# Performance work log

Measured on AMD Instinct MI355X. Metric: run time of the kernel, lower is better.

## Reference

```python
import jax, jax.numpy as jnp
import numpy as np

B, T, D, H = 8, 1024, 1024, 16
HD = D // H
SCALE = HD ** -0.5


def setup_inputs() -> dict:
    key = jax.random.key(0)
    ks = jax.random.split(key, 5)
    s = 0.02
    return {
        "hidden_states": jax.random.normal(ks[0], (B, T, D), jnp.float32),
        "Wq": jax.random.normal(ks[1], (D, D), jnp.float32) * s,
        "bq": jnp.zeros((D,), jnp.float32),
        "Wk": jax.random.normal(ks[2], (D, D), jnp.float32) * s,
        "bk": jnp.zeros((D,), jnp.float32),
        "Wv": jax.random.normal(ks[3], (D, D), jnp.float32) * s,
        "bv": jnp.zeros((D,), jnp.float32),
        "Wo": jax.random.normal(ks[4], (D, D), jnp.float32) * s,
        "bo": jnp.zeros((D,), jnp.float32),
    }


def _split_heads(x):
    # [B, T, D] -> [B, H, T, HD]
    return x.reshape(B, T, H, HD).transpose(0, 2, 1, 3)


def reference(hidden_states, Wq, bq, Wk, bk, Wv, bv, Wo, bo):
    q = _split_heads((hidden_states @ Wq + bq) * SCALE)
    k = _split_heads(hidden_states @ Wk + bk)
    v = _split_heads(hidden_states @ Wv + bv)
    # [B, H, T, T] attention scores
    scores = jnp.einsum("bhqd,bhkd->bhqk", q, k)
    probs = jax.nn.softmax(scores, axis=-1)
    attn = jnp.einsum("bhqk,bhkd->bhqd", probs, v)
    attn = attn.transpose(0, 2, 1, 3).reshape(B, T, D)
    return attn @ Wo + bo
```

## Files before the change

kernel.cpp:

```cpp
#include <hip/hip_runtime.h>

typedef unsigned short u16;
typedef __attribute__((ext_vector_type(4))) float f32x4;
typedef __attribute__((ext_vector_type(8))) __bf16 bf16x8;
typedef __attribute__((ext_vector_type(4))) __bf16 bf16x4;
typedef __attribute__((ext_vector_type(4))) unsigned short u16x4;
typedef __attribute__((ext_vector_type(8))) unsigned short u16x8;

static __device__ __forceinline__ u16 f2bf(float f) {
    union { float f; unsigned u; } v; v.f = f;
    unsigned r = v.u + 0x7FFFu + ((v.u >> 16) & 1u);
    return (u16)(r >> 16);
}

static __device__ __forceinline__ float exp2f_fast(float x) {
    float r; asm("v_exp_f32 %0, %1" : "=v"(r) : "v"(x)); return r;
}

static __device__ __forceinline__ void gload16(const u16* g, u16* l) {
    __builtin_amdgcn_global_load_lds(
        (const __attribute__((address_space(1))) unsigned int*)g,
        (__attribute__((address_space(3))) unsigned int*)l, 16, 0, 0);
}

template<int N> static __device__ __forceinline__ void vm_wait() {
    if constexpr (N >= 8)      asm volatile("s_waitcnt vmcnt(8)" ::: "memory");
    else if constexpr (N == 6) asm volatile("s_waitcnt vmcnt(6)" ::: "memory");
    else if constexpr (N == 4) asm volatile("s_waitcnt vmcnt(4)" ::: "memory");
    else if constexpr (N == 3) asm volatile("s_waitcnt vmcnt(3)" ::: "memory");
    else                       asm volatile("s_waitcnt vmcnt(0)" ::: "memory");
}

#define SWZ64(row, ec) (((row) * 64) + ((((ec) ^ ((row) & 7))) << 3))

__global__ __launch_bounds__(256) void k_cvt(const float* __restrict__ in, u16* __restrict__ out) {
    size_t i = (size_t)blockIdx.x * 256 + threadIdx.x;
    float4 v = ((const float4*)in)[i];
    u16x4 o; o[0] = f2bf(v.x); o[1] = f2bf(v.y); o[2] = f2bf(v.z); o[3] = f2bf(v.w);
    *(u16x4*)(out + i * 4) = o;
}

__global__ __launch_bounds__(256) void k_wtrans4(
    const float* __restrict__ W0, const float* __restrict__ W1,
    const float* __restrict__ W2, const float* __restrict__ W3,
    u16* __restrict__ T0, u16* __restrict__ T1, u16* __restrict__ T2, u16* __restrict__ T3,
    float s0) {
    const float* W; u16* Tt; float sc;
    switch (blockIdx.z) {
        case 0:  W = W0; Tt = T0; sc = s0;  break;
        case 1:  W = W1; Tt = T1; sc = 1.f; break;
        case 2:  W = W2; Tt = T2; sc = 1.f; break;
        default: W = W3; Tt = T3; sc = 1.f; break;
    }
    __shared__ float tile[32][33];
    int n0 = blockIdx.x * 32, k0 = blockIdx.y * 32;
    int tid = threadIdx.x;
    int r = tid >> 3, c = (tid & 7) * 4;
    float4 v = *(const float4*)(W + (size_t)(k0 + r) * 1024 + n0 + c);
    tile[r][c] = v.x; tile[r][c + 1] = v.y; tile[r][c + 2] = v.z; tile[r][c + 3] = v.w;
    __syncthreads();
    u16x4 o;
    o[0] = f2bf(tile[c][r] * sc);
    o[1] = f2bf(tile[c + 1][r] * sc);
    o[2] = f2bf(tile[c + 2][r] * sc);
    o[3] = f2bf(tile[c + 3][r] * sc);
    *(u16x4*)(Tt + (size_t)(n0 + r) * 1024 + k0 + c) = o;
}

template<int BN>
__global__ __launch_bounds__(512, 2) void k_g256(
    const u16* __restrict__ A, const u16* __restrict__ Bt,
    const float* __restrict__ bias, const float* __restrict__ biasK, float qscale,
    u16* __restrict__ obf, u16* __restrict__ obK, float* __restrict__ of32,
    int ldc, int bias_row, int nblk, int mode) {
    constexpr int WN = (BN == 256) ? 4 : 2;
    constexpr int WAVE_M = (BN == 256) ? 128 : 64;
    constexpr int M_REP = WAVE_M / 16;
    constexpr int ABUF = 256 * 64;
    constexpr int BBUF = BN * 64;
    __shared__ u16 As[2 * ABUF];
    __shared__ u16 Bs[2 * BBUF];
    const int tid = threadIdx.x;
    const int l = tid & 63, w = tid >> 6;
    const int mw = w / WN, nw = w % WN;
    const int fr = l & 15, gg = l >> 4, f4 = gg * 4;
    const int id = blockIdx.x;
    const int swz = (id & 7) * 32 + (id >> 3);
    const int bm = swz / nblk, bn = swz % nblk;
    const size_t m0 = (size_t)bm * 256, n0v = (size_t)bn * BN;

    const int strow = tid >> 3;
    const int sch = ((tid & 7) ^ (strow & 7)) * 8;
    const u16* Ag = A + (m0 + strow) * 1024 + sch;
    const u16* Bg = Bt + (n0v + strow) * 1024 + sch;
    const int ldst = tid * 8;

    const int kc0 = (gg ^ (fr & 7)) << 3;
    const int abase = (mw * WAVE_M + fr) * 64;
    const int bbase = (nw * 64 + fr) * 64;

    f32x4 acc[M_REP][4] = {};

#define SA(c, J, b) gload16(Ag + (size_t)(c) * 65536 + (size_t)(J) * 64, As + (b) * ABUF + (c) * 4096 + ldst);
#define SB(c, J, b) gload16(Bg + (size_t)(c) * 65536 + (size_t)(J) * 64, Bs + (b) * BBUF + (c) * 4096 + ldst);
#define PH_BAR()                                                        \
    __builtin_amdgcn_s_barrier();                                       \
    asm volatile("s_waitcnt lgkmcnt(0)" ::: "memory");                  \
    __builtin_amdgcn_sched_barrier(0)
#define MFMA16(AB)                                                      \
    __builtin_amdgcn_s_setprio(1);                                      \
    _Pragma("unroll")                                                   \
    for (int mt = 0; mt < 4; ++mt)                                      \
        _Pragma("unroll")                                               \
        for (int nt = 0; nt < 4; ++nt)                                  \
            acc[(AB) + mt][nt] = __builtin_amdgcn_mfma_f32_16x16x32_bf16(afr[mt], bfr[nt], acc[(AB) + mt][nt], 0, 0, 0); \
    __builtin_amdgcn_s_setprio(0)

    SA(0, 0, 0) SA(1, 0, 0) SA(2, 0, 0) SA(3, 0, 0)
    SB(0, 0, 0) SB(1, 0, 0)
    if constexpr (BN == 256) { SB(2, 0, 0) SB(3, 0, 0) }

#define GT256(b, J, STG)                                                                      \
    {                                                                                         \
        asm volatile("s_waitcnt vmcnt(0)" ::: "memory");                                      \
        __builtin_amdgcn_s_barrier();                                                         \
        bf16x8 bfr[4], afr[4];                                                                \
        _Pragma("unroll")                                                                     \
        for (int nt = 0; nt < 4; ++nt) bfr[nt] = *(const bf16x8*)(&Bs[(b) * BBUF + bbase + nt * 1024 + kc0]); \
        _Pragma("unroll")                                                                     \
        for (int mt = 0; mt < 4; ++mt) afr[mt] = *(const bf16x8*)(&As[(b) * ABUF + abase + mt * 1024 + kc0]); \
        if (STG) { SA(0, (J) + 1, (b) ^ 1) SA(1, (J) + 1, (b) ^ 1) }                          \
        PH_BAR();                                                                             \
        MFMA16(0);                                                                            \
        _Pragma("unroll")                                                                     \
        for (int mt = 0; mt < 4; ++mt) afr[mt] = *(const bf16x8*)(&As[(b) * ABUF + abase + (mt + 4) * 1024 + kc0]); \
        if (STG) { SA(2, (J) + 1, (b) ^ 1) SA(3, (J) + 1, (b) ^ 1) }                          \
        PH_BAR();                                                                             \
        MFMA16(4);                                                                            \
        _Pragma("unroll")                                                                     \
        for (int nt = 0; nt < 4; ++nt) bfr[nt] = *(const bf16x8*)(&Bs[(b) * BBUF + bbase + nt * 1024 + (kc0 ^ 32)]); \
        _Pragma("unroll")                                                                     \
        for (int mt = 0; mt < 4; ++mt) afr[mt] = *(const bf16x8*)(&As[(b) * ABUF + abase + mt * 1024 + (kc0 ^ 32)]); \
        if (STG) { SB(0, (J) + 1, (b) ^ 1) SB(1, (J) + 1, (b) ^ 1) }                          \
        PH_BAR();                                                                             \
        MFMA16(0);                                                                            \
        _Pragma("unroll")                                                                     \
        for (int mt = 0; mt < 4; ++mt) afr[mt] = *(const bf16x8*)(&As[(b) * ABUF + abase + (mt + 4) * 1024 + (kc0 ^ 32)]); \
        if (STG) { SB(2, (J) + 1, (b) ^ 1) SB(3, (J) + 1, (b) ^ 1) }                          \
        PH_BAR();                                                                             \
        MFMA16(4);                                                                            \
    }

#define GT128(b, J, STG)                                                                      \
    {                                                                                         \
        asm volatile("s_waitcnt vmcnt(0)" ::: "memory");                                      \
        __builtin_amdgcn_s_barrier();                                                         \
        bf16x8 bfr[4], afr[4];                                                                \
        _Pragma("unroll")                                                                     \
        for (int nt = 0; nt < 4; ++nt) bfr[nt] = *(const bf16x8*)(&Bs[(b) * BBUF + bbase + nt * 1024 + kc0]); \
        _Pragma("unroll")                                                                     \
        for (int mt = 0; mt < 4; ++mt) afr[mt] = *(const bf16x8*)(&As[(b) * ABUF + abase + mt * 1024 + kc0]); \
        if (STG) { SA(0, (J) + 1, (b) ^ 1) SA(1, (J) + 1, (b) ^ 1) SB(0, (J) + 1, (b) ^ 1) }  \
        PH_BAR();                                                                             \
        MFMA16(0);                                                                            \
        _Pragma("unroll")                                                                     \
        for (int nt = 0; nt < 4; ++nt) bfr[nt] = *(const bf16x8*)(&Bs[(b) * BBUF + bbase + nt * 1024 + (kc0 ^ 32)]); \
        _Pragma("unroll")                                                                     \
        for (int mt = 0; mt < 4; ++mt) afr[mt] = *(const bf16x8*)(&As[(b) * ABUF + abase + mt * 1024 + (kc0 ^ 32)]); \
        if (STG) { SA(2, (J) + 1, (b) ^ 1) SA(3, (J) + 1, (b) ^ 1) SB(1, (J) + 1, (b) ^ 1) }  \
        PH_BAR();                                                                             \
        MFMA16(0);                                                                            \
    }

    if constexpr (BN == 256) {
#pragma unroll 1
        for (int j = 0; j < 14; j += 2) { GT256(0, j, 1) GT256(1, j + 1, 1) }
        GT256(0, 14, 1) GT256(1, 15, 0)
    } else {
#pragma unroll 1
        for (int j = 0; j < 14; j += 2) { GT128(0, j, 1) GT128(1, j + 1, 1) }
        GT128(0, 14, 1) GT128(1, 15, 0)
    }
#undef GT256
#undef GT128
#undef SA
#undef SB
#undef PH_BAR
#undef MFMA16

    const int mrow0 = (int)m0 + mw * WAVE_M;
    const int ncol0 = (int)n0v + nw * 64;
    if (mode == 1) {
#pragma unroll
        for (int mt = 0; mt < M_REP; ++mt)
#pragma unroll
            for (int nt = 0; nt < 4; ++nt) {
                const int col = ncol0 + nt * 16 + fr;
                const int seg = col >> 10, colm = col & 1023;
                const float bb = (seg ? biasK[colm] : bias[colm] * qscale);
                u16* op = seg ? obK : obf;
#pragma unroll
                for (int r = 0; r < 4; ++r)
                    op[(size_t)(mrow0 + mt * 16 + f4 + r) * 1024 + colm] = f2bf(acc[mt][nt][r] + bb);
            }
    } else if (mode == 2) {
#pragma unroll
        for (int mt = 0; mt < M_REP; ++mt) {
            float rb_[4];
#pragma unroll
            for (int r = 0; r < 4; ++r) rb_[r] = bias[mrow0 + mt * 16 + f4 + r];
#pragma unroll
            for (int nt = 0; nt < 4; ++nt) {
                const int col = ncol0 + nt * 16 + fr;
                const int colp = (col & ~31) | (((col >> 2) & 3) << 3) |
                                 (((col >> 4) & 1) << 2) | (col & 3);
#pragma unroll
                for (int r = 0; r < 4; ++r) {
                    const size_t row = (size_t)(mrow0 + mt * 16 + f4 + r);
                    obf[row * (size_t)ldc + colp] = f2bf(acc[mt][nt][r] + rb_[r]);
                }
            }
        }
    } else {
#pragma unroll
        for (int mt = 0; mt < M_REP; ++mt) {
            float rb_[4];
#pragma unroll
            for (int r = 0; r < 4; ++r)
                rb_[r] = bias_row ? bias[mrow0 + mt * 16 + f4 + r] : 0.f;
#pragma unroll
            for (int nt = 0; nt < 4; ++nt) {
                const int col = ncol0 + nt * 16 + fr;
                const float cb = bias_row ? 0.f : bias[col];
#pragma unroll
                for (int r = 0; r < 4; ++r) {
                    const size_t row = (size_t)(mrow0 + mt * 16 + f4 + r);
                    const float vv = acc[mt][nt][r] + cb + rb_[r];
                    if (of32) of32[row * (size_t)ldc + col] = vv;
                    else      obf[row * (size_t)ldc + col] = f2bf(vv);
                }
            }
        }
    }
}

static __device__ __forceinline__ void qk_tile(const u16* Ks, int fr, int gg,
                                               bf16x8 qA0, bf16x8 qA1, bf16x8 qB0, bf16x8 qB1,
                                               float mA, float mB, f32x4 sA[4], f32x4 sB[4]) {
    __builtin_amdgcn_s_setprio(1);
#pragma unroll
    for (int nt = 0; nt < 4; ++nt) {
        const int rk = nt * 16 + fr;
        const bf16x8 kf0 = *(const bf16x8*)(&Ks[SWZ64(rk, gg)]);
        const bf16x8 kf1 = *(const bf16x8*)(&Ks[SWZ64(rk, gg + 4)]);
        f32x4 z = {-mA, -mA, -mA, -mA};
        z = __builtin_amdgcn_mfma_f32_16x16x32_bf16(kf0, qA0, z, 0, 0, 0);
        z = __builtin_amdgcn_mfma_f32_16x16x32_bf16(kf1, qA1, z, 0, 0, 0);
        sA[nt] = z;
        f32x4 y = {-mB, -mB, -mB, -mB};
        y = __builtin_amdgcn_mfma_f32_16x16x32_bf16(kf0, qB0, y, 0, 0, 0);
        y = __builtin_amdgcn_mfma_f32_16x16x32_bf16(kf1, qB1, y, 0, 0, 0);
        sB[nt] = y;
    }
    __builtin_amdgcn_s_setprio(0);
}

static __device__ __forceinline__ void sm_tile(const f32x4 s[4], f32x4 o[4],
                                               float& m, float& lsum, bf16x4 p[4]) {
    float mymax = s[0][0];
#pragma unroll
    for (int nt = 0; nt < 4; ++nt)
#pragma unroll
        for (int r = 0; r < 4; ++r) mymax = fmaxf(mymax, s[nt][r]);
    float ps = 0.f;
#pragma unroll
    for (int nt = 0; nt < 4; ++nt)
#pragma unroll
        for (int r = 0; r < 4; ++r) {
            const float pp = exp2f_fast(s[nt][r]);
            ps += pp; p[nt][r] = (__bf16)pp;
        }
    if (__builtin_expect(__any(mymax > 11.0f), 0)) {
        float rm = fmaxf(mymax, __shfl_xor(mymax, 16, 64));
        rm = fmaxf(rm, __shfl_xor(rm, 32, 64));
        const float d = fmaxf(rm, 0.f);
        const float fac = exp2f_fast(-d);
        m += d; lsum *= fac;
#pragma unroll
        for (int mt = 0; mt < 4; ++mt)
#pragma unroll
            for (int r = 0; r < 4; ++r) o[mt][r] *= fac;
        ps = 0.f;
#pragma unroll
        for (int nt = 0; nt < 4; ++nt)
#pragma unroll
            for (int r = 0; r < 4; ++r) {
                const float pp = exp2f_fast(s[nt][r] - d);
                ps += pp; p[nt][r] = (__bf16)pp;
            }
    }
    lsum += ps;
}

static __device__ __forceinline__ void pv_tile(const u16* Vs, int fr, int gg,
                                               const bf16x4 pA[4], const bf16x4 pB[4],
                                               f32x4 oA[4], f32x4 oB[4]) {
    const bf16x8 BA0 = __builtin_shufflevector(pA[0], pA[1], 0, 1, 2, 3, 4, 5, 6, 7);
    const bf16x8 BA1 = __builtin_shufflevector(pA[2], pA[3], 0, 1, 2, 3, 4, 5, 6, 7);
    const bf16x8 BB0 = __builtin_shufflevector(pB[0], pB[1], 0, 1, 2, 3, 4, 5, 6, 7);
    const bf16x8 BB1 = __builtin_shufflevector(pB[2], pB[3], 0, 1, 2, 3, 4, 5, 6, 7);
    __builtin_amdgcn_s_setprio(1);
#pragma unroll
    for (int mt = 0; mt < 4; ++mt) {
        const int rv = mt * 16 + fr;
        const bf16x8 vk0 = *(const bf16x8*)(&Vs[SWZ64(rv, gg)]);
        const bf16x8 vk1 = *(const bf16x8*)(&Vs[SWZ64(rv, gg + 4)]);
        oA[mt] = __builtin_amdgcn_mfma_f32_16x16x32_bf16(vk0, BA0, oA[mt], 0, 0, 0);
        oA[mt] = __builtin_amdgcn_mfma_f32_16x16x32_bf16(vk1, BA1, oA[mt], 0, 0, 0);
        oB[mt] = __builtin_amdgcn_mfma_f32_16x16x32_bf16(vk0, BB0, oB[mt], 0, 0, 0);
        oB[mt] = __builtin_amdgcn_mfma_f32_16x16x32_bf16(vk1, BB1, oB[mt], 0, 0, 0);
    }
    __builtin_amdgcn_s_setprio(0);
}

__global__ __launch_bounds__(256, 2) void k_flash(const u16* __restrict__ Q, const u16* __restrict__ K,
                                                  const u16* __restrict__ Vt2, u16* __restrict__ O) {
    __shared__ u16 Ks[4][64 * 64];
    __shared__ u16 Vs[4][64 * 64];
    const int tid = threadIdx.x;
    const int l = tid & 63, w = tid >> 6;
    const int id = blockIdx.x;
    const int swz = (id & 7) * 128 + (id >> 3);
    const int bh = swz >> 3, qt = swz & 7;
    const int b = bh >> 4, h = bh & 15;
    const int qw = qt * 128 + w * 32;
    const int fr = l & 15, gg = l >> 4, f4 = gg * 4, f8 = gg * 8;

    const u16* qpA = Q + ((size_t)(b * 1024 + qw + fr)) * 1024 + h * 64 + f8;
    const u16* qpB = qpA + 16 * 1024;
    const bf16x8 qA0 = *(const bf16x8*)qpA;
    const bf16x8 qA1 = *(const bf16x8*)(qpA + 32);
    const bf16x8 qB0 = *(const bf16x8*)qpB;
    const bf16x8 qB1 = *(const bf16x8*)(qpB + 32);

    const int jj0 = w * 2, jj1 = w * 2 + 1;
    const int sr0 = jj0 * 8 + (l >> 3), sr1 = jj1 * 8 + (l >> 3);
    const int sc = ((l & 7) ^ (l >> 3)) * 8;
    const u16* kg0 = K + ((size_t)(b * 1024 + sr0)) * 1024 + h * 64 + sc;
    const u16* kg1 = K + ((size_t)(b * 1024 + sr1)) * 1024 + h * 64 + sc;
    const u16* vg0 = Vt2 + ((size_t)(h * 64 + sr0)) * 8192 + b * 1024 + sc;
    const u16* vg1 = Vt2 + ((size_t)(h * 64 + sr1)) * 8192 + b * 1024 + sc;
    const int lk0 = jj0 * 512 + l * 8, lk1 = jj1 * 512 + l * 8;

#define FSTG(S, kt)                                         \
    gload16(kg0 + (size_t)(kt) * 1024, Ks[S] + lk0);        \
    gload16(kg1 + (size_t)(kt) * 1024, Ks[S] + lk1);        \
    gload16(vg0 + (kt), Vs[S] + lk0);                       \
    gload16(vg1 + (kt), Vs[S] + lk1);

    f32x4 oA[4] = {}, oB[4] = {};
    float mA = 0.f, lA = 0.f, mB = 0.f, lB = 0.f;
    bf16x4 p0A[4], p0B[4], p1A[4], p1B[4];

    FSTG(0, 0) FSTG(1, 64)

#define FITER(T, PCA, PCB, PPA, PPB, VMN, DOPV)                              \
    {                                                                        \
        vm_wait<VMN>();                                                      \
        __builtin_amdgcn_s_barrier();                                        \
        f32x4 sA[4], sB[4];                                                  \
        qk_tile(Ks[(T) & 3], fr, gg, qA0, qA1, qB0, qB1, mA, mB, sA, sB);    \
        if ((T) + 2 <= 15) { FSTG((((T) + 2) & 3), ((T) + 2) * 64) }         \
        if (DOPV) pv_tile(Vs[((T) - 1) & 3], fr, gg, PPA, PPB, oA, oB);      \
        sm_tile(sA, oA, mA, lA, PCA);                                        \
        sm_tile(sB, oB, mB, lB, PCB);                                        \
    }

    FITER(0,  p0A, p0B, p1A, p1B, 4, false)
    FITER(1,  p1A, p1B, p0A, p0B, 4, true)
    FITER(2,  p0A, p0B, p1A, p1B, 4, true)
    FITER(3,  p1A, p1B, p0A, p0B, 4, true)
    FITER(4,  p0A, p0B, p1A, p1B, 4, true)
    FITER(5,  p1A, p1B, p0A, p0B, 4, true)
    FITER(6,  p0A, p0B, p1A, p1B, 4, true)
    FITER(7,  p1A, p1B, p0A, p0B, 4, true)
    FITER(8,  p0A, p0B, p1A, p1B, 4, true)
    FITER(9,  p1A, p1B, p0A, p0B, 4, true)
    FITER(10, p0A, p0B, p1A, p1B, 4, true)
    FITER(11, p1A, p1B, p0A, p0B, 4, true)
    FITER(12, p0A, p0B, p1A, p1B, 4, true)
    FITER(13, p1A, p1B, p0A, p0B, 4, true)
    FITER(14, p0A, p0B, p1A, p1B, 4, true)
    FITER(15, p1A, p1B, p0A, p0B, 0, true)
#undef FITER
#undef FSTG
    pv_tile(Vs[3], fr, gg, p1A, p1B, oA, oB);

    lA += __shfl_xor(lA, 16, 64); lA += __shfl_xor(lA, 32, 64);
    lB += __shfl_xor(lB, 16, 64); lB += __shfl_xor(lB, 32, 64);
    const float ivA = 1.0f / lA, ivB = 1.0f / lB;
    u16* opA = O + ((size_t)(b * 1024 + qw + fr)) * 1024 + h * 64;
    u16* opB = opA + 16 * 1024;
#pragma unroll
    for (int mt = 0; mt < 4; ++mt) {
        u16x4 oa, ob;
#pragma unroll
        for (int r = 0; r < 4; ++r) { oa[r] = f2bf(oA[mt][r] * ivA); ob[r] = f2bf(oB[mt][r] * ivB); }
        *(u16x4*)(opA + mt * 16 + f4) = oa;
        *(u16x4*)(opB + mt * 16 + f4) = ob;
    }
}

extern "C" void kernel_launch(void* const* d_in, const int* in_sizes, int n_in,
                              void* d_out, int out_size, void* d_ws, size_t ws_size,
                              hipStream_t stream) {
    (void)in_sizes; (void)n_in; (void)out_size; (void)ws_size;
    const float* hs = (const float*)d_in[0];
    const float* Wq = (const float*)d_in[1];
    const float* bq = (const float*)d_in[2];
    const float* Wk = (const float*)d_in[3];
    const float* bk = (const float*)d_in[4];
    const float* Wv = (const float*)d_in[5];
    const float* bv = (const float*)d_in[6];
    const float* Wo = (const float*)d_in[7];
    const float* bo = (const float*)d_in[8];
    float* out = (float*)d_out;
    char* ws = (char*)d_ws;
    const size_t MB = 1024ull * 1024ull;
    u16* Xb  = (u16*)(ws);
    u16* Wqt = (u16*)(ws + 16 * MB);
    u16* Wkt = (u16*)(ws + 18 * MB);
    u16* Wvt = (u16*)(ws + 20 * MB);
    u16* Wot = (u16*)(ws + 22 * MB);
    u16* Qb  = (u16*)(ws + 24 * MB);
    u16* Kb  = (u16*)(ws + 40 * MB);
    u16* Vt2 = (u16*)(ws + 56 * MB);
    u16* Ob  = Xb;

    const float SCALE_Q = 0.125f * 1.4426950408889634f;

    k_cvt<<<dim3(8192), dim3(256), 0, stream>>>(hs, Xb);
    k_wtrans4<<<dim3(32, 32, 4), dim3(256), 0, stream>>>(Wq, Wk, Wv, Wo, Wqt, Wkt, Wvt, Wot, SCALE_Q);
    k_g256<256><<<dim3(256), dim3(512), 0, stream>>>(Xb, Wqt, bq, bk, SCALE_Q,
                                                     Qb, Kb, nullptr, 1024, 0, 8, 1);
    k_g256<128><<<dim3(256), dim3(512), 0, stream>>>(Wvt, Xb, bv, nullptr, 1.f,
                                                     Vt2, nullptr, nullptr, 8192, 1, 64, 2);
    k_flash<<<dim3(1024), dim3(256), 0, stream>>>(Qb, Kb, Vt2, Ob);
    k_g256<128><<<dim3(256), dim3(512), 0, stream>>>(Ob, Wot, bo, nullptr, 1.f,
                                                     nullptr, nullptr, out, 1024, 0, 8, 0);
}
```

Measured before the change: 153.7 us.

## Split GEMM K-tiles into half planes and stagger K/V loads in flash

The projection GEMM now stores each 64-wide K tile as two 32-wide LDS planes with a new swizzle. It waits only for the first half-plane before starting MFMAs, using partial vmcnt waits in place of a full vmcnt(0) drain. The flash attention kernel cuts its K/V ring from four stages to three and loads V one tile later than K, which lowers LDS use and lets loads overlap compute. The risks are subtle waitcnt and buffer-index mistakes, plus the 32-wide plane layout changing LDS bank behaviour.

```diff
diff --git a/kernel.cpp b/kernel.cpp
--- a/kernel.cpp
+++ b/kernel.cpp
@@ -28,6 +28,7 @@
     else if constexpr (N == 6) asm volatile("s_waitcnt vmcnt(6)" ::: "memory");
     else if constexpr (N == 4) asm volatile("s_waitcnt vmcnt(4)" ::: "memory");
     else if constexpr (N == 3) asm volatile("s_waitcnt vmcnt(3)" ::: "memory");
+    else if constexpr (N == 2) asm volatile("s_waitcnt vmcnt(2)" ::: "memory");
     else                       asm volatile("s_waitcnt vmcnt(0)" ::: "memory");
 }
 
@@ -76,8 +77,10 @@
     constexpr int WN = (BN == 256) ? 4 : 2;
     constexpr int WAVE_M = (BN == 256) ? 128 : 64;
     constexpr int M_REP = WAVE_M / 16;
-    constexpr int ABUF = 256 * 64;
-    constexpr int BBUF = BN * 64;
+    constexpr int APLANE = 256 * 32;
+    constexpr int ABUF = 2 * APLANE;
+    constexpr int BPLANE = BN * 32;
+    constexpr int BBUF = 2 * BPLANE;
     __shared__ u16 As[2 * ABUF];
     __shared__ u16 Bs[2 * BBUF];
     const int tid = threadIdx.x;
@@ -89,21 +92,21 @@
     const int bm = swz / nblk, bn = swz % nblk;
     const size_t m0 = (size_t)bm * 256, n0v = (size_t)bn * BN;
 
-    const int strow = tid >> 3;
-    const int sch = ((tid & 7) ^ (strow & 7)) * 8;
-    const u16* Ag = A + (m0 + strow) * 1024 + sch;
-    const u16* Bg = Bt + (n0v + strow) * 1024 + sch;
-    const int ldst = tid * 8;
-
-    const int kc0 = (gg ^ (fr & 7)) << 3;
-    const int abase = (mw * WAVE_M + fr) * 64;
-    const int bbase = (nw * 64 + fr) * 64;
+    const u16* AgS = A + (m0 + (tid >> 2)) * 1024 + ((tid & 3) ^ ((tid >> 3) & 3)) * 8;
+    const u16* BgS = Bt + (n0v + (tid >> 2)) * 1024 + ((tid & 3) ^ ((tid >> 3) & 3)) * 8;
+    const int t8 = tid * 8;
+
+    const int kcsw = (gg ^ ((fr >> 1) & 3)) * 8;
+    const int arow = mw * WAVE_M + fr;
+    const int brow = nw * 64 + fr;
 
     f32x4 acc[M_REP][4] = {};
 
-#define SA(c, J, b) gload16(Ag + (size_t)(c) * 65536 + (size_t)(J) * 64, As + (b) * ABUF + (c) * 4096 + ldst);
-#define SB(c, J, b) gload16(Bg + (size_t)(c) * 65536 + (size_t)(J) * 64, Bs + (b) * BBUF + (c) * 4096 + ldst);
-#define PH_BAR()                                                        \
+#define SA(hr, kh, TJ, b) gload16(AgS + (hr) * 131072 + (TJ) * 64 + (kh) * 32, \
+                                  As + (b) * ABUF + (kh) * APLANE + (hr) * 4096 + t8);
+#define SB(hr, kh, TJ, b) gload16(BgS + (hr) * 131072 + (TJ) * 64 + (kh) * 32, \
+                                  Bs + (b) * BBUF + (kh) * BPLANE + (hr) * 4096 + t8);
+#define PH_END()                                                        \
     __builtin_amdgcn_s_barrier();                                       \
     asm volatile("s_waitcnt lgkmcnt(0)" ::: "memory");                  \
     __builtin_amdgcn_sched_barrier(0)
@@ -116,76 +119,84 @@
             acc[(AB) + mt][nt] = __builtin_amdgcn_mfma_f32_16x16x32_bf16(afr[mt], bfr[nt], acc[(AB) + mt][nt], 0, 0, 0); \
     __builtin_amdgcn_s_setprio(0)
 
-    SA(0, 0, 0) SA(1, 0, 0) SA(2, 0, 0) SA(3, 0, 0)
-    SB(0, 0, 0) SB(1, 0, 0)
-    if constexpr (BN == 256) { SB(2, 0, 0) SB(3, 0, 0) }
-
-#define GT256(b, J, STG)                                                                      \
+    if constexpr (BN == 256) {
+        SA(0, 0, 0, 0) SA(1, 0, 0, 0) SB(0, 0, 0, 0) SB(1, 0, 0, 0)
+        SA(0, 1, 0, 0) SA(1, 1, 0, 0) SB(0, 1, 0, 0) SB(1, 1, 0, 0)
+    } else {
+        SA(0, 0, 0, 0) SA(1, 0, 0, 0) SB(0, 0, 0, 0)
+        SA(0, 1, 0, 0) SA(1, 1, 0, 0) SB(0, 1, 0, 0)
+    }
+
+#define GT256(b, J, STG, VM3)                                                                 \
     {                                                                                         \
-        asm volatile("s_waitcnt vmcnt(0)" ::: "memory");                                      \
+        vm_wait<4>();                                                                         \
         __builtin_amdgcn_s_barrier();                                                         \
         bf16x8 bfr[4], afr[4];                                                                \
         _Pragma("unroll")                                                                     \
-        for (int nt = 0; nt < 4; ++nt) bfr[nt] = *(const bf16x8*)(&Bs[(b) * BBUF + bbase + nt * 1024 + kc0]); \
-        _Pragma("unroll")                                                                     \
-        for (int mt = 0; mt < 4; ++mt) afr[mt] = *(const bf16x8*)(&As[(b) * ABUF + abase + mt * 1024 + kc0]); \
-        if (STG) { SA(0, (J) + 1, (b) ^ 1) SA(1, (J) + 1, (b) ^ 1) }                          \
-        PH_BAR();                                                                             \
+        for (int nt = 0; nt < 4; ++nt) bfr[nt] = *(const bf16x8*)(&Bs[(b) * BBUF + (brow + nt * 16) * 32 + kcsw]); \
+        _Pragma("unroll")                                                                     \
+        for (int mt = 0; mt < 4; ++mt) afr[mt] = *(const bf16x8*)(&As[(b) * ABUF + (arow + mt * 16) * 32 + kcsw]); \
+        if (STG) { SA(0, 0, (J) + 1, (b) ^ 1) SA(1, 0, (J) + 1, (b) ^ 1) }                    \
+        PH_END();                                                                             \
         MFMA16(0);                                                                            \
         _Pragma("unroll")                                                                     \
-        for (int mt = 0; mt < 4; ++mt) afr[mt] = *(const bf16x8*)(&As[(b) * ABUF + abase + (mt + 4) * 1024 + kc0]); \
-        if (STG) { SA(2, (J) + 1, (b) ^ 1) SA(3, (J) + 1, (b) ^ 1) }                          \
-        PH_BAR();                                                                             \
+        for (int mt = 0; mt < 4; ++mt) afr[mt] = *(const bf16x8*)(&As[(b) * ABUF + (arow + (mt + 4) * 16) * 32 + kcsw]); \
+        if (STG) { SB(0, 0, (J) + 1, (b) ^ 1) SB(1, 0, (J) + 1, (b) ^ 1) }                    \
+        PH_END();                                                                             \
         MFMA16(4);                                                                            \
-        _Pragma("unroll")                                                                     \
-        for (int nt = 0; nt < 4; ++nt) bfr[nt] = *(const bf16x8*)(&Bs[(b) * BBUF + bbase + nt * 1024 + (kc0 ^ 32)]); \
-        _Pragma("unroll")                                                                     \
-        for (int mt = 0; mt < 4; ++mt) afr[mt] = *(const bf16x8*)(&As[(b) * ABUF + abase + mt * 1024 + (kc0 ^ 32)]); \
-        if (STG) { SB(0, (J) + 1, (b) ^ 1) SB(1, (J) + 1, (b) ^ 1) }                          \
-        PH_BAR();                                                                             \
+        vm_wait<VM3>();                                                                       \
+        __builtin_amdgcn_s_barrier();                                                         \
+        _Pragma("unroll")                                                                     \
+        for (int nt = 0; nt < 4; ++nt) bfr[nt] = *(const bf16x8*)(&Bs[(b) * BBUF + BPLANE + (brow + nt * 16) * 32 + kcsw]); \
+        _Pragma("unroll")                                                                     \
+        for (int mt = 0; mt < 4; ++mt) afr[mt] = *(const bf16x8*)(&As[(b) * ABUF + APLANE + (arow + mt * 16) * 32 + kcsw]); \
+        if (STG) { SA(0, 1, (J) + 1, (b) ^ 1) SA(1, 1, (J) + 1, (b) ^ 1) }                    \
+        PH_END();                                                                             \
         MFMA16(0);                                                                            \
         _Pragma("unroll")                                                                     \
-        for (int mt = 0; mt < 4; ++mt) afr[mt] = *(const bf16x8*)(&As[(b) * ABUF + abase + (mt + 4) * 1024 + (kc0 ^ 32)]); \
-        if (STG) { SB(2, (J) + 1, (b) ^ 1) SB(3, (J) + 1, (b) ^ 1) }                          \
-        PH_BAR();                                                                             \
+        for (int mt = 0; mt < 4; ++mt) afr[mt] = *(const bf16x8*)(&As[(b) * ABUF + APLANE + (arow + (mt + 4) * 16) * 32 + kcsw]); \
+        if (STG) { SB(0, 1, (J) + 1, (b) ^ 1) SB(1, 1, (J) + 1, (b) ^ 1) }                    \
+        PH_END();                                                                             \
         MFMA16(4);                                                                            \
     }
 
-#define GT128(b, J, STG)                                                                      \
+#define GT128(b, J, STG, VM2)                                                                 \
     {                                                                                         \
-        asm volatile("s_waitcnt vmcnt(0)" ::: "memory");                                      \
+        vm_wait<3>();                                                                         \
         __builtin_amdgcn_s_barrier();                                                         \
         bf16x8 bfr[4], afr[4];                                                                \
         _Pragma("unroll")                                                                     \
-        for (int nt = 0; nt < 4; ++nt) bfr[nt] = *(const bf16x8*)(&Bs[(b) * BBUF + bbase + nt * 1024 + kc0]); \
-        _Pragma("unroll")                                                                     \
-        for (int mt = 0; mt < 4; ++mt) afr[mt] = *(const bf16x8*)(&As[(b) * ABUF + abase + mt * 1024 + kc0]); \
-        if (STG) { SA(0, (J) + 1, (b) ^ 1) SA(1, (J) + 1, (b) ^ 1) SB(0, (J) + 1, (b) ^ 1) }  \
-        PH_BAR();                                                                             \
+        for (int nt = 0; nt < 4; ++nt) bfr[nt] = *(const bf16x8*)(&Bs[(b) * BBUF + (brow + nt * 16) * 32 + kcsw]); \
+        _Pragma("unroll")                                                                     \
+        for (int mt = 0; mt < 4; ++mt) afr[mt] = *(const bf16x8*)(&As[(b) * ABUF + (arow + mt * 16) * 32 + kcsw]); \
+        if (STG) { SA(0, 0, (J) + 1, (b) ^ 1) SA(1, 0, (J) + 1, (b) ^ 1) SB(0, 0, (J) + 1, (b) ^ 1) } \
+        PH_END();                                                                             \
         MFMA16(0);                                                                            \
-        _Pragma("unroll")                                                                     \
-        for (int nt = 0; nt < 4; ++nt) bfr[nt] = *(const bf16x8*)(&Bs[(b) * BBUF + bbase + nt * 1024 + (kc0 ^ 32)]); \
-        _Pragma("unroll")                                                                     \
-        for (int mt = 0; mt < 4; ++mt) afr[mt] = *(const bf16x8*)(&As[(b) * ABUF + abase + mt * 1024 + (kc0 ^ 32)]); \
-        if (STG) { SA(2, (J) + 1, (b) ^ 1) SA(3, (J) + 1, (b) ^ 1) SB(1, (J) + 1, (b) ^ 1) }  \
-        PH_BAR();                                                                             \
+        vm_wait<VM2>();                                                                       \
+        __builtin_amdgcn_s_barrier();                                                         \
+        _Pragma("unroll")                                                                     \
+        for (int nt = 0; nt < 4; ++nt) bfr[nt] = *(const bf16x8*)(&Bs[(b) * BBUF + BPLANE + (brow + nt * 16) * 32 + kcsw]); \
+        _Pragma("unroll")                                                                     \
+        for (int mt = 0; mt < 4; ++mt) afr[mt] = *(const bf16x8*)(&As[(b) * ABUF + APLANE + (arow + mt * 16) * 32 + kcsw]); \
+        if (STG) { SA(0, 1, (J) + 1, (b) ^ 1) SA(1, 1, (J) + 1, (b) ^ 1) SB(0, 1, (J) + 1, (b) ^ 1) } \
+        PH_END();                                                                             \
         MFMA16(0);                                                                            \
     }
 
     if constexpr (BN == 256) {
 #pragma unroll 1
-        for (int j = 0; j < 14; j += 2) { GT256(0, j, 1) GT256(1, j + 1, 1) }
-        GT256(0, 14, 1) GT256(1, 15, 0)
+        for (int j = 0; j < 14; j += 2) { GT256(0, j, 1, 4) GT256(1, j + 1, 1, 4) }
+        GT256(0, 14, 1, 4) GT256(1, 15, 0, 0)
     } else {
 #pragma unroll 1
-        for (int j = 0; j < 14; j += 2) { GT128(0, j, 1) GT128(1, j + 1, 1) }
-        GT128(0, 14, 1) GT128(1, 15, 0)
+        for (int j = 0; j < 14; j += 2) { GT128(0, j, 1, 3) GT128(1, j + 1, 1, 3) }
+        GT128(0, 14, 1, 3) GT128(1, 15, 0, 0)
     }
 #undef GT256
 #undef GT128
 #undef SA
 #undef SB
-#undef PH_BAR
+#undef PH_END
 #undef MFMA16
 
     const int mrow0 = (int)m0 + mw * WAVE_M;
@@ -325,8 +336,8 @@
 
 __global__ __launch_bounds__(256, 2) void k_flash(const u16* __restrict__ Q, const u16* __restrict__ K,
                                                   const u16* __restrict__ Vt2, u16* __restrict__ O) {
-    __shared__ u16 Ks[4][64 * 64];
-    __shared__ u16 Vs[4][64 * 64];
+    __shared__ u16 Ks[3][64 * 64];
+    __shared__ u16 Vs[3][64 * 64];
     const int tid = threadIdx.x;
     const int l = tid & 63, w = tid >> 6;
     const int id = blockIdx.x;
@@ -352,9 +363,10 @@
     const u16* vg1 = Vt2 + ((size_t)(h * 64 + sr1)) * 8192 + b * 1024 + sc;
     const int lk0 = jj0 * 512 + l * 8, lk1 = jj1 * 512 + l * 8;
 
-#define FSTG(S, kt)                                         \
+#define FSTGK(S, kt)                                        \
     gload16(kg0 + (size_t)(kt) * 1024, Ks[S] + lk0);        \
-    gload16(kg1 + (size_t)(kt) * 1024, Ks[S] + lk1);        \
+    gload16(kg1 + (size_t)(kt) * 1024, Ks[S] + lk1);
+#define FSTGV(S, kt)                                        \
     gload16(vg0 + (kt), Vs[S] + lk0);                       \
     gload16(vg1 + (kt), Vs[S] + lk1);
 
@@ -362,39 +374,43 @@
     float mA = 0.f, lA = 0.f, mB = 0.f, lB = 0.f;
     bf16x4 p0A[4], p0B[4], p1A[4], p1B[4];
 
-    FSTG(0, 0) FSTG(1, 64)
-
-#define FITER(T, PCA, PCB, PPA, PPB, VMN, DOPV)                              \
+    FSTGK(0, 0) FSTGK(1, 64) FSTGV(0, 0)
+
+#define FITER(T, QS, PS, KS, VS, PCA, PCB, PPA, PPB, VMN, DOPV, DOK, DOV)    \
     {                                                                        \
         vm_wait<VMN>();                                                      \
         __builtin_amdgcn_s_barrier();                                        \
         f32x4 sA[4], sB[4];                                                  \
-        qk_tile(Ks[(T) & 3], fr, gg, qA0, qA1, qB0, qB1, mA, mB, sA, sB);    \
-        if ((T) + 2 <= 15) { FSTG((((T) + 2) & 3), ((T) + 2) * 64) }         \
-        if (DOPV) pv_tile(Vs[((T) - 1) & 3], fr, gg, PPA, PPB, oA, oB);      \
+        qk_tile(Ks[QS], fr, gg, qA0, qA1, qB0, qB1, mA, mB, sA, sB);         \
+        if (DOK) { FSTGK(KS, ((T) + 2) * 64) }                               \
+        if (DOV) { FSTGV(VS, ((T) + 1) * 64) }                               \
+        if (DOPV) pv_tile(Vs[PS], fr, gg, PPA, PPB, oA, oB);                 \
         sm_tile(sA, oA, mA, lA, PCA);                                        \
         sm_tile(sB, oB, mB, lB, PCB);                                        \
     }
 
-    FITER(0,  p0A, p0B, p1A, p1B, 4, false)
-    FITER(1,  p1A, p1B, p0A, p0B, 4, true)
-    FITER(2,  p0A, p0B, p1A, p1B, 4, true)
-    FITER(3,  p1A, p1B, p0A, p0B, 4, true)
-    FITER(4,  p0A, p0B, p1A, p1B, 4, true)
-    FITER(5,  p1A, p1B, p0A, p0B, 4, true)
-    FITER(6,  p0A, p0B, p1A, p1B, 4, true)
-    FITER(7,  p1A, p1B, p0A, p0B, 4, true)
-    FITER(8,  p0A, p0B, p1A, p1B, 4, true)
-    FITER(9,  p1A, p1B, p0A, p0B, 4, true)
-    FITER(10, p0A, p0B, p1A, p1B, 4, true)
-    FITER(11, p1A, p1B, p0A, p0B, 4, true)
-    FITER(12, p0A, p0B, p1A, p1B, 4, true)
-    FITER(13, p1A, p1B, p0A, p0B, 4, true)
-    FITER(14, p0A, p0B, p1A, p1B, 4, true)
-    FITER(15, p1A, p1B, p0A, p0B, 0, true)
+    FITER(0,  0, 0, 2, 1, p0A, p0B, p1A, p1B, 4, 0, 1, 1)
+    FITER(1,  1, 0, 0, 2, p1A, p1B, p0A, p0B, 4, 1, 1, 1)
+    FITER(2,  2, 1, 1, 0, p0A, p0B, p1A, p1B, 4, 1, 1, 1)
+    FITER(3,  0, 2, 2, 1, p1A, p1B, p0A, p0B, 4, 1, 1, 1)
+    FITER(4,  1, 0, 0, 2, p0A, p0B, p1A, p1B, 4, 1, 1, 1)
+    FITER(5,  2, 1, 1, 0, p1A, p1B, p0A, p0B, 4, 1, 1, 1)
+    FITER(6,  0, 2, 2, 1, p0A, p0B, p1A, p1B, 4, 1, 1, 1)
+    FITER(7,  1, 0, 0, 2, p1A, p1B, p0A, p0B, 4, 1, 1, 1)
+    FITER(8,  2, 1, 1, 0, p0A, p0B, p1A, p1B, 4, 1, 1, 1)
+    FITER(9,  0, 2, 2, 1, p1A, p1B, p0A, p0B, 4, 1, 1, 1)
+    FITER(10, 1, 0, 0, 2, p0A, p0B, p1A, p1B, 4, 1, 1, 1)
+    FITER(11, 2, 1, 1, 0, p1A, p1B, p0A, p0B, 4, 1, 1, 1)
+    FITER(12, 0, 2, 2, 1, p0A, p0B, p1A, p1B, 4, 1, 1, 1)
+    FITER(13, 1, 0, 0, 2, p1A, p1B, p0A, p0B, 4, 1, 1, 1)
+    FITER(14, 2, 1, 0, 0, p0A, p0B, p1A, p1B, 4, 1, 0, 1)
+    FITER(15, 0, 2, 0, 0, p1A, p1B, p0A, p0B, 2, 1, 0, 0)
 #undef FITER
-#undef FSTG
-    pv_tile(Vs[3], fr, gg, p1A, p1B, oA, oB);
+    vm_wait<0>();
+    __builtin_amdgcn_s_barrier();
+    pv_tile(Vs[0], fr, gg, p1A, p1B, oA, oB);
+#undef FSTGK
+#undef FSTGV
 
     lA += __shfl_xor(lA, 16, 64); lA += __shfl_xor(lA, 32, 64);
     lB += __shfl_xor(lB, 16, 64); lB += __shfl_xor(lB, 32, 64);
```

Measured after the change: 155.3 us. No clear change (+1.0%).
